# Performance work log

Hardware: AMD Instinct MI355X
Metric: run time of the kernel (lower is better)

## Reference

```python
import jax, jax.numpy as jnp
import numpy as np

B, S, H = 4, 256, 8
N_MB, N_C = 50000, 1000
P, BS, CS, L0, L1, L2 = 32, 16, 16, 96, 32, 16


def setup_inputs() -> dict:
    key = jax.random.key(0)
    ks = jax.random.split(key, 12)
    sd = 0.02
    return {
        "attention_scores": jax.random.normal(ks[0], (B, H, S, S), dtype=jnp.float32),
        "b_seq": jax.random.randint(ks[1], (B, S), 0, N_MB + 1, dtype=jnp.int32),
        "c_seq": jax.random.randint(ks[2], (B, S), 0, N_C + 2, dtype=jnp.int32),
        "e_pos": jax.random.normal(ks[3], (S * 2, H, P), dtype=jnp.float32) * sd,
        "e_bi": jax.random.normal(ks[4], (N_MB + 1, H, BS), dtype=jnp.float32) * sd,
        "e_bj": jax.random.normal(ks[5], (N_MB + 1, H, BS), dtype=jnp.float32) * sd,
        "e_ci": jax.random.normal(ks[6], (N_C + 2, H, CS), dtype=jnp.float32) * sd,
        "e_cj": jax.random.normal(ks[7], (N_C + 2, H, CS), dtype=jnp.float32) * sd,
        "w1_e": jax.random.normal(ks[8], (L0, L1, H), dtype=jnp.float32) * sd,
        "w2_e": jax.random.normal(ks[9], (L1, L2, H), dtype=jnp.float32) * sd,
        "w3_e": jax.random.normal(ks[10], (L2, H), dtype=jnp.float32) * sd,
    }


def reference(attention_scores, b_seq, c_seq, e_pos, e_bi, e_bj, e_ci, e_cj, w1_e, w2_e, w3_e):
    b, h, s, _ = attention_scores.shape
    pos = jnp.arange(s, dtype=jnp.int32)
    # relative position index (i - j + seq_len), shared across batch: [S,S]
    f_pos = pos[:, None] - pos[None, :] + s
    emb_pos = e_pos[f_pos]                 # [S,S,H,P]
    emb_bi = e_bi[b_seq]                   # [B,S,H,BS]
    emb_bj = e_bj[b_seq]
    emb_ci = e_ci[c_seq]                   # [B,S,H,CS]
    emb_cj = e_cj[c_seq]
    # concat of broadcasted features -> e: [B,S,S,H,L0]
    e = jnp.concatenate([
        jnp.broadcast_to(emb_pos[None], (b, s, s, h, emb_pos.shape[-1])),
        jnp.broadcast_to(emb_bi[:, :, None], (b, s, s, h, emb_bi.shape[-1])),
        jnp.broadcast_to(emb_bj[:, None, :], (b, s, s, h, emb_bj.shape[-1])),
        jnp.broadcast_to(emb_ci[:, :, None], (b, s, s, h, emb_ci.shape[-1])),
        jnp.broadcast_to(emb_cj[:, None, :], (b, s, s, h, emb_cj.shape[-1])),
    ], axis=-1)
    e1 = jax.nn.relu(jnp.einsum('bmnhd,dkh->bmnhk', e, w1_e))
    e2 = jax.nn.relu(jnp.einsum('bmnhk,klh->bmnhl', e1, w2_e))
    da_score = jnp.einsum('bmnhk,kh->bhmn', e2, w3_e)
    return attention_scores + da_score
```

## Files before the change

### kernel.cpp

```cpp
#include <hip/hip_runtime.h>
#include <stdint.h>

typedef __attribute__((ext_vector_type(8))) short short8;
typedef __attribute__((ext_vector_type(4))) float f32x4;

#define SEQ 256
#define NH 8

__device__ __forceinline__ uint32_t cvt_pk_bf16(float lo, float hi) {
  uint32_t r;
  asm("v_cvt_pk_bf16_f32 %0, %1, %2" : "=v"(r) : "v"(lo), "v"(hi));
  return r;
}

__device__ __forceinline__ short8 pack8(f32x4 a, f32x4 b) {
  union { uint32_t u[4]; short8 v; } t;
  t.u[0] = cvt_pk_bf16(a[0], a[1]);
  t.u[1] = cvt_pk_bf16(a[2], a[3]);
  t.u[2] = cvt_pk_bf16(b[0], b[1]);
  t.u[3] = cvt_pk_bf16(b[2], b[3]);
  return t.v;
}

__global__ __launch_bounds__(256) void build_tables_mfma(
    const int* __restrict__ bseq, const int* __restrict__ cseq,
    const float* __restrict__ epos, const float* __restrict__ ebi,
    const float* __restrict__ ebj, const float* __restrict__ eci,
    const float* __restrict__ ecj, const float* __restrict__ w1,
    float* __restrict__ Tpos, float* __restrict__ Ti, float* __restrict__ Tj) {
  int lane = threadIdx.x & 63, w = threadIdx.x >> 6;
  int task = blockIdx.x * 4 + w;
  int lcol = lane & 15, kb = lane >> 4, k8 = kb * 8;
  f32x4 zero = {0.f, 0.f, 0.f, 0.f};

  if (task < 256) {
    int h = task >> 5, ft = task & 31;
    short8 bf[2];
#pragma unroll
    for (int kt = 0; kt < 2; ++kt) {
      union { uint32_t u[4]; short8 v; } t;
#pragma unroll
      for (int r = 0; r < 4; ++r) {
        float lo = w1[(k8 + 2 * r) * 256 + (kt * 16 + lcol) * 8 + h];
        float hi = w1[(k8 + 2 * r + 1) * 256 + (kt * 16 + lcol) * 8 + h];
        t.u[r] = cvt_pk_bf16(lo, hi);
      }
      bf[kt] = t.v;
    }
    const float* ep = epos + ((ft * 16 + lcol) * NH + h) * 32 + k8;
    short8 af = pack8(*(const f32x4*)ep, *(const f32x4*)(ep + 4));
#pragma unroll
    for (int kt = 0; kt < 2; ++kt) {
      f32x4 d = __builtin_amdgcn_mfma_f32_16x16x32_bf16(af, bf[kt], zero, 0, 0, 0);
#pragma unroll
      for (int r = 0; r < 4; ++r)
        Tpos[h * 16384 + (ft * 16 + kb * 4 + r) * 32 + kt * 16 + lcol] = d[r];
    }
  } else {
    int isI = task < 768;
    int t2 = task - (isI ? 256 : 768);
    int h = t2 >> 6, bm = t2 & 63;
    int p0 = isI ? ((kb < 2 ? 32 : 48) + k8)
                 : ((kb < 2 ? 48 : 64) + k8);
    short8 bf[2];
#pragma unroll
    for (int kt = 0; kt < 2; ++kt) {
      union { uint32_t u[4]; short8 v; } t;
#pragma unroll
      for (int r = 0; r < 4; ++r) {
        float lo = w1[(p0 + 2 * r) * 256 + (kt * 16 + lcol) * 8 + h];
        float hi = w1[(p0 + 2 * r + 1) * 256 + (kt * 16 + lcol) * 8 + h];
        t.u[r] = cvt_pk_bf16(lo, hi);
      }
      bf[kt] = t.v;
    }
    int gm = bm * 16 + lcol;
    int bi = bseq[gm], ci = cseq[gm];
    const float* eB = isI ? ebi : ebj;
    const float* eC = isI ? eci : ecj;
    const float* src = (kb < 2) ? eB + (bi * NH + h) * 16 + k8
                                : eC + (ci * NH + h) * 16 + (k8 - 16);
    short8 af = pack8(*(const f32x4*)src, *(const f32x4*)(src + 4));
    float* T = isI ? Ti : Tj;
#pragma unroll
    for (int kt = 0; kt < 2; ++kt) {
      f32x4 d = __builtin_amdgcn_mfma_f32_16x16x32_bf16(af, bf[kt], zero, 0, 0, 0);
#pragma unroll
      for (int r = 0; r < 4; ++r)
        T[h * 32768 + (bm * 16 + kb * 4 + r) * 32 + kt * 16 + lcol] = d[r];
    }
  }
}

__global__ __launch_bounds__(512, 4) void dis_att_main(
    const float* __restrict__ attn, const float* __restrict__ w2,
    const float* __restrict__ w3, const float* __restrict__ Tpos,
    const float* __restrict__ Ti, const float* __restrict__ Tj,
    float* __restrict__ out) {
  __shared__ float sAp[127][36];
  __shared__ float sAi[64][36];
  __shared__ float sAj[64][36];
  int tid = threadIdx.x;
  int wg = blockIdx.x;
  int nt = wg & 3, mt = (wg >> 2) & 3, h = (wg >> 4) & 7, b = wg >> 7;
  int m0 = mt * 64, n0 = nt * 64;
  int f0 = m0 - n0 + 193;

  {
    int r = tid >> 3, q = tid & 7;
    const float* P = Tpos + h * 16384 + (f0 + r) * 32 + q * 4;
    *(f32x4*)&sAp[r][q * 4] = *(const f32x4*)P;
    if (r + 64 < 127)
      *(f32x4*)&sAp[r + 64][q * 4] = *(const f32x4*)(P + 64 * 32);
    *(f32x4*)&sAi[r][q * 4] =
        *(const f32x4*)(Ti + h * 32768 + (b * 256 + m0 + r) * 32 + q * 4);
    *(f32x4*)&sAj[r][q * 4] =
        *(const f32x4*)(Tj + h * 32768 + (b * 256 + n0 + r) * 32 + q * 4);
  }
  __syncthreads();

  int lane = tid & 63, w = tid >> 6;
  int lcol = lane & 15, kb = lane >> 4, k8 = kb * 8;
  f32x4 zero = {0.f, 0.f, 0.f, 0.f};

  union { uint32_t u[4]; short8 v; } w2f;
#pragma unroll
  for (int r = 0; r < 4; ++r) {
    float lo = w2[(k8 + 2 * r) * 128 + lcol * 8 + h];
    float hi = w2[(k8 + 2 * r + 1) * 128 + lcol * 8 + h];
    w2f.u[r] = cvt_pk_bf16(lo, hi);
  }
  float w3v[4];
#pragma unroll
  for (int r = 0; r < 4; ++r) w3v[r] = w3[(kb * 4 + r) * 8 + h];

  f32x4 ajA[4], ajB[4];
#pragma unroll
  for (int ng = 0; ng < 4; ++ng) {
    int nl = ng * 16 + lcol;
    ajA[ng] = *(const f32x4*)&sAj[nl][k8];
    ajB[ng] = *(const f32x4*)&sAj[nl][k8 + 4];
  }

  const float* attn_b = attn + (b * NH + h) * SEQ * SEQ;
  float* out_b = out + (b * NH + h) * SEQ * SEQ;
  int bit4 = kb & 1, bit5 = kb & 2;

#pragma unroll
  for (int s = 0; s < 2; ++s) {
    int mb = w * 8 + s * 4;
    float av[4];
    int idxs[4];
#pragma unroll
    for (int ng = 0; ng < 4; ++ng) {
      idxs[ng] = (m0 + mb + kb) * SEQ + n0 + ng * 16 + lcol;
      av[ng] = attn_b[idxs[ng]];
    }
    f32x4 aiA[4], aiB[4];
#pragma unroll
    for (int mi = 0; mi < 4; ++mi) {
      aiA[mi] = *(const f32x4*)&sAi[mb + mi][k8];
      aiB[mi] = *(const f32x4*)&sAi[mb + mi][k8 + 4];
    }
#pragma unroll
    for (int ng = 0; ng < 4; ++ng) {
      int nl = ng * 16 + lcol;
      f32x4 pA[4], pB[4];
#pragma unroll
      for (int mi = 0; mi < 4; ++mi) {
        int rl = mb + mi - nl + 63;
        pA[mi] = *(const f32x4*)&sAp[rl][k8];
        pB[mi] = *(const f32x4*)&sAp[rl][k8 + 4];
      }
      __builtin_amdgcn_sched_barrier(0);
      float part[4];
#pragma unroll
      for (int mi = 0; mi < 4; ++mi) {
        f32x4 s0 = pA[mi] + aiA[mi] + ajA[ng];
        f32x4 s1 = pB[mi] + aiB[mi] + ajB[ng];
        union { uint32_t u[4]; short8 v; } ef;
        ef.u[0] = cvt_pk_bf16(fmaxf(s0[0], 0.f), fmaxf(s0[1], 0.f));
        ef.u[1] = cvt_pk_bf16(fmaxf(s0[2], 0.f), fmaxf(s0[3], 0.f));
        ef.u[2] = cvt_pk_bf16(fmaxf(s1[0], 0.f), fmaxf(s1[1], 0.f));
        ef.u[3] = cvt_pk_bf16(fmaxf(s1[2], 0.f), fmaxf(s1[3], 0.f));
        f32x4 d = __builtin_amdgcn_mfma_f32_16x16x32_bf16(w2f.v, ef.v, zero, 0, 0, 0);
        part[mi] = fmaxf(d[0], 0.f) * w3v[0] + fmaxf(d[1], 0.f) * w3v[1] +
                   fmaxf(d[2], 0.f) * w3v[2] + fmaxf(d[3], 0.f) * w3v[3];
      }
      float mineA = bit4 ? part[1] : part[0];
      float sendA = bit4 ? part[0] : part[1];
      float mineB = bit4 ? part[3] : part[2];
      float sendB = bit4 ? part[2] : part[3];
      mineA += __shfl_xor(sendA, 16, 64);
      mineB += __shfl_xor(sendB, 16, 64);
      float keep = bit5 ? mineB : mineA;
      float send = bit5 ? mineA : mineB;
      float res = keep + __shfl_xor(send, 32, 64);
      out_b[idxs[ng]] = av[ng] + res;
    }
  }
}

extern "C" void kernel_launch(void* const* d_in, const int* in_sizes, int n_in,
                              void* d_out, int out_size, void* d_ws, size_t ws_size,
                              hipStream_t stream) {
  const float* attn = (const float*)d_in[0];
  const int* bseq   = (const int*)d_in[1];
  const int* cseq   = (const int*)d_in[2];
  const float* epos = (const float*)d_in[3];
  const float* ebi  = (const float*)d_in[4];
  const float* ebj  = (const float*)d_in[5];
  const float* eci  = (const float*)d_in[6];
  const float* ecj  = (const float*)d_in[7];
  const float* w1   = (const float*)d_in[8];
  const float* w2   = (const float*)d_in[9];
  const float* w3   = (const float*)d_in[10];
  float* out = (float*)d_out;

  float* Tpos = (float*)d_ws;
  float* Ti   = Tpos + 131072;
  float* Tj   = Ti + 262144;

  hipLaunchKernelGGL(build_tables_mfma, dim3(320), dim3(256), 0, stream,
                     bseq, cseq, epos, ebi, ebj, eci, ecj, w1, Tpos, Ti, Tj);
  hipLaunchKernelGGL(dis_att_main, dim3(512), dim3(512), 0, stream,
                     attn, w2, w3, Tpos, Ti, Tj, out);
}
```

Before: 25.66 us.

## Double-buffer positional LDS loads and use permlane swaps for lane reductions

Prefetches the next column group's positional table rows from LDS into a second register buffer while the current group's MFMAs run, replacing the sched_barrier that serialized the loads. The cross-lane reduction now uses permlane16/32 swap builtins, when available, to fully reduce each of the four partial sums instead of the select-and-shuffle scheme. Launch bounds are relaxed to 2 blocks per SM, allowing more registers for the extra buffer at the cost of occupancy. The full reductions do more adds and permutes per output than the previous butterfly scheme.

```diff
diff --git a/kernel.cpp b/kernel.cpp
--- a/kernel.cpp
+++ b/kernel.cpp
@@ -20,6 +20,27 @@
   t.u[2] = cvt_pk_bf16(b[0], b[1]);
   t.u[3] = cvt_pk_bf16(b[2], b[3]);
   return t.v;
+}
+
+__device__ __forceinline__ float xorsum16(float x) {
+#if __has_builtin(__builtin_amdgcn_permlane16_swap)
+  unsigned ux = __builtin_bit_cast(unsigned, x);
+  auto r = __builtin_amdgcn_permlane16_swap(ux, ux, false, false);
+  return __builtin_bit_cast(float, (unsigned)r[0]) +
+         __builtin_bit_cast(float, (unsigned)r[1]);
+#else
+  return x + __shfl_xor(x, 16, 64);
+#endif
+}
+__device__ __forceinline__ float xorsum32(float x) {
+#if __has_builtin(__builtin_amdgcn_permlane32_swap)
+  unsigned ux = __builtin_bit_cast(unsigned, x);
+  auto r = __builtin_amdgcn_permlane32_swap(ux, ux, false, false);
+  return __builtin_bit_cast(float, (unsigned)r[0]) +
+         __builtin_bit_cast(float, (unsigned)r[1]);
+#else
+  return x + __shfl_xor(x, 32, 64);
+#endif
 }
 
 __global__ __launch_bounds__(256) void build_tables_mfma(
@@ -92,7 +113,7 @@
   }
 }
 
-__global__ __launch_bounds__(512, 4) void dis_att_main(
+__global__ __launch_bounds__(512, 2) void dis_att_main(
     const float* __restrict__ attn, const float* __restrict__ w2,
     const float* __restrict__ w3, const float* __restrict__ Tpos,
     const float* __restrict__ Ti, const float* __restrict__ Tj,
@@ -162,22 +183,30 @@
       aiA[mi] = *(const f32x4*)&sAi[mb + mi][k8];
       aiB[mi] = *(const f32x4*)&sAi[mb + mi][k8 + 4];
     }
+    f32x4 pA[2][4], pB[2][4];
+#pragma unroll
+    for (int mi = 0; mi < 4; ++mi) {
+      int rl = mb + mi - lcol + 63;
+      pA[0][mi] = *(const f32x4*)&sAp[rl][k8];
+      pB[0][mi] = *(const f32x4*)&sAp[rl][k8 + 4];
+    }
 #pragma unroll
     for (int ng = 0; ng < 4; ++ng) {
-      int nl = ng * 16 + lcol;
-      f32x4 pA[4], pB[4];
+      int cur = ng & 1, nxt = cur ^ 1;
+      if (ng < 3) {
+        int nl2 = (ng + 1) * 16 + lcol;
+#pragma unroll
+        for (int mi = 0; mi < 4; ++mi) {
+          int rl = mb + mi - nl2 + 63;
+          pA[nxt][mi] = *(const f32x4*)&sAp[rl][k8];
+          pB[nxt][mi] = *(const f32x4*)&sAp[rl][k8 + 4];
+        }
+      }
+      float part[4];
 #pragma unroll
       for (int mi = 0; mi < 4; ++mi) {
-        int rl = mb + mi - nl + 63;
-        pA[mi] = *(const f32x4*)&sAp[rl][k8];
-        pB[mi] = *(const f32x4*)&sAp[rl][k8 + 4];
-      }
-      __builtin_amdgcn_sched_barrier(0);
-      float part[4];
-#pragma unroll
-      for (int mi = 0; mi < 4; ++mi) {
-        f32x4 s0 = pA[mi] + aiA[mi] + ajA[ng];
-        f32x4 s1 = pB[mi] + aiB[mi] + ajB[ng];
+        f32x4 s0 = pA[cur][mi] + aiA[mi] + ajA[ng];
+        f32x4 s1 = pB[cur][mi] + aiB[mi] + ajB[ng];
         union { uint32_t u[4]; short8 v; } ef;
         ef.u[0] = cvt_pk_bf16(fmaxf(s0[0], 0.f), fmaxf(s0[1], 0.f));
         ef.u[1] = cvt_pk_bf16(fmaxf(s0[2], 0.f), fmaxf(s0[3], 0.f));
@@ -187,16 +216,14 @@
         part[mi] = fmaxf(d[0], 0.f) * w3v[0] + fmaxf(d[1], 0.f) * w3v[1] +
                    fmaxf(d[2], 0.f) * w3v[2] + fmaxf(d[3], 0.f) * w3v[3];
       }
-      float mineA = bit4 ? part[1] : part[0];
-      float sendA = bit4 ? part[0] : part[1];
-      float mineB = bit4 ? part[3] : part[2];
-      float sendB = bit4 ? part[2] : part[3];
-      mineA += __shfl_xor(sendA, 16, 64);
-      mineB += __shfl_xor(sendB, 16, 64);
-      float keep = bit5 ? mineB : mineA;
-      float send = bit5 ? mineA : mineB;
-      float res = keep + __shfl_xor(send, 32, 64);
-      out_b[idxs[ng]] = av[ng] + res;
+      float S0 = xorsum32(xorsum16(part[0]));
+      float S1 = xorsum32(xorsum16(part[1]));
+      float S2 = xorsum32(xorsum16(part[2]));
+      float S3 = xorsum32(xorsum16(part[3]));
+      float p01 = bit4 ? S1 : S0;
+      float p23 = bit4 ? S3 : S2;
+      float pf = bit5 ? p23 : p01;
+      out_b[idxs[ng]] = av[ng] + pf;
     }
   }
 }
```

After: 28.70 us. 1.12x slower.

## Store first-layer tables as packed fp16 in LDS and use packed-half add/relu

Applied to the files above, without the earlier changes.

The main kernel now converts the precomputed position/i/j first-layer tables to fp16 when staging them into shared memory, which halves LDS footprint and read traffic. The per-element combine becomes packed f16 adds and a packed max instead of fp32 adds followed by bf16 conversion. The second-layer MFMA switches from bf16 to f16 inputs. This cuts VALU conversion work and LDS reads in the inner loop, at the cost of fp16 rounding and range in the summed hidden activations.

```diff
diff --git a/kernel.cpp b/kernel.cpp
--- a/kernel.cpp
+++ b/kernel.cpp
@@ -2,7 +2,9 @@
 #include <stdint.h>
 
 typedef __attribute__((ext_vector_type(8))) short short8;
+typedef __attribute__((ext_vector_type(8))) _Float16 half8;
 typedef __attribute__((ext_vector_type(4))) float f32x4;
+typedef __attribute__((ext_vector_type(4))) uint32_t u32x4;
 
 #define SEQ 256
 #define NH 8
@@ -10,6 +12,21 @@
 __device__ __forceinline__ uint32_t cvt_pk_bf16(float lo, float hi) {
   uint32_t r;
   asm("v_cvt_pk_bf16_f32 %0, %1, %2" : "=v"(r) : "v"(lo), "v"(hi));
+  return r;
+}
+__device__ __forceinline__ uint32_t cvt_pk_f16(float lo, float hi) {
+  uint32_t r;
+  asm("v_cvt_pkrtz_f16_f32 %0, %1, %2" : "=v"(r) : "v"(lo), "v"(hi));
+  return r;
+}
+__device__ __forceinline__ uint32_t pk_add(uint32_t a, uint32_t b) {
+  uint32_t r;
+  asm("v_pk_add_f16 %0, %1, %2" : "=v"(r) : "v"(a), "v"(b));
+  return r;
+}
+__device__ __forceinline__ uint32_t pk_relu(uint32_t a) {
+  uint32_t r;
+  asm("v_pk_max_f16 %0, %1, 0" : "=v"(r) : "v"(a));
   return r;
 }
 
@@ -97,9 +114,9 @@
     const float* __restrict__ w3, const float* __restrict__ Tpos,
     const float* __restrict__ Ti, const float* __restrict__ Tj,
     float* __restrict__ out) {
-  __shared__ float sAp[127][36];
-  __shared__ float sAi[64][36];
-  __shared__ float sAj[64][36];
+  __shared__ uint32_t sApB[127][20];
+  __shared__ uint32_t sAiB[64][20];
+  __shared__ uint32_t sAjB[64][20];
   int tid = threadIdx.x;
   int wg = blockIdx.x;
   int nt = wg & 3, mt = (wg >> 2) & 3, h = (wg >> 4) & 7, b = wg >> 7;
@@ -107,40 +124,54 @@
   int f0 = m0 - n0 + 193;
 
   {
-    int r = tid >> 3, q = tid & 7;
-    const float* P = Tpos + h * 16384 + (f0 + r) * 32 + q * 4;
-    *(f32x4*)&sAp[r][q * 4] = *(const f32x4*)P;
-    if (r + 64 < 127)
-      *(f32x4*)&sAp[r + 64][q * 4] = *(const f32x4*)(P + 64 * 32);
-    *(f32x4*)&sAi[r][q * 4] =
-        *(const f32x4*)(Ti + h * 32768 + (b * 256 + m0 + r) * 32 + q * 4);
-    *(f32x4*)&sAj[r][q * 4] =
-        *(const f32x4*)(Tj + h * 32768 + (b * 256 + n0 + r) * 32 + q * 4);
+    int r = tid >> 1, q = tid & 1;
+    const float* src = nullptr;
+    uint32_t* dst = nullptr;
+    if (r < 127) {
+      src = Tpos + h * 16384 + (f0 + r) * 32;
+      dst = &sApB[r][0];
+    } else if (r < 191) {
+      src = Ti + h * 32768 + (b * 256 + m0 + (r - 127)) * 32;
+      dst = &sAiB[r - 127][0];
+    } else if (r < 255) {
+      src = Tj + h * 32768 + (b * 256 + n0 + (r - 191)) * 32;
+      dst = &sAjB[r - 191][0];
+    }
+    if (src) {
+      const float* s16 = src + q * 16;
+      f32x4 v0 = *(const f32x4*)s16;
+      f32x4 v1 = *(const f32x4*)(s16 + 4);
+      f32x4 v2 = *(const f32x4*)(s16 + 8);
+      f32x4 v3 = *(const f32x4*)(s16 + 12);
+      u32x4 o0 = {cvt_pk_f16(v0[0], v0[1]), cvt_pk_f16(v0[2], v0[3]),
+                  cvt_pk_f16(v1[0], v1[1]), cvt_pk_f16(v1[2], v1[3])};
+      u32x4 o1 = {cvt_pk_f16(v2[0], v2[1]), cvt_pk_f16(v2[2], v2[3]),
+                  cvt_pk_f16(v3[0], v3[1]), cvt_pk_f16(v3[2], v3[3])};
+      *(u32x4*)(dst + q * 8) = o0;
+      *(u32x4*)(dst + q * 8 + 4) = o1;
+    }
   }
   __syncthreads();
 
   int lane = tid & 63, w = tid >> 6;
-  int lcol = lane & 15, kb = lane >> 4, k8 = kb * 8;
+  int lcol = lane & 15, kb = lane >> 4, k8 = kb * 8, kq = kb * 4;
   f32x4 zero = {0.f, 0.f, 0.f, 0.f};
 
-  union { uint32_t u[4]; short8 v; } w2f;
+  union { uint32_t u[4]; half8 v; } w2f;
 #pragma unroll
   for (int r = 0; r < 4; ++r) {
     float lo = w2[(k8 + 2 * r) * 128 + lcol * 8 + h];
     float hi = w2[(k8 + 2 * r + 1) * 128 + lcol * 8 + h];
-    w2f.u[r] = cvt_pk_bf16(lo, hi);
+    w2f.u[r] = cvt_pk_f16(lo, hi);
   }
   float w3v[4];
 #pragma unroll
   for (int r = 0; r < 4; ++r) w3v[r] = w3[(kb * 4 + r) * 8 + h];
 
-  f32x4 ajA[4], ajB[4];
-#pragma unroll
-  for (int ng = 0; ng < 4; ++ng) {
-    int nl = ng * 16 + lcol;
-    ajA[ng] = *(const f32x4*)&sAj[nl][k8];
-    ajB[ng] = *(const f32x4*)&sAj[nl][k8 + 4];
-  }
+  u32x4 ajP[4];
+#pragma unroll
+  for (int ng = 0; ng < 4; ++ng)
+    ajP[ng] = *(const u32x4*)&sAjB[ng * 16 + lcol][kq];
 
   const float* attn_b = attn + (b * NH + h) * SEQ * SEQ;
   float* out_b = out + (b * NH + h) * SEQ * SEQ;
@@ -156,34 +187,26 @@
       idxs[ng] = (m0 + mb + kb) * SEQ + n0 + ng * 16 + lcol;
       av[ng] = attn_b[idxs[ng]];
     }
-    f32x4 aiA[4], aiB[4];
-#pragma unroll
-    for (int mi = 0; mi < 4; ++mi) {
-      aiA[mi] = *(const f32x4*)&sAi[mb + mi][k8];
-      aiB[mi] = *(const f32x4*)&sAi[mb + mi][k8 + 4];
-    }
+    u32x4 aiP[4];
+#pragma unroll
+    for (int mi = 0; mi < 4; ++mi)
+      aiP[mi] = *(const u32x4*)&sAiB[mb + mi][kq];
 #pragma unroll
     for (int ng = 0; ng < 4; ++ng) {
       int nl = ng * 16 + lcol;
-      f32x4 pA[4], pB[4];
-#pragma unroll
-      for (int mi = 0; mi < 4; ++mi) {
-        int rl = mb + mi - nl + 63;
-        pA[mi] = *(const f32x4*)&sAp[rl][k8];
-        pB[mi] = *(const f32x4*)&sAp[rl][k8 + 4];
-      }
+      u32x4 pP[4];
+#pragma unroll
+      for (int mi = 0; mi < 4; ++mi)
+        pP[mi] = *(const u32x4*)&sApB[mb + mi - nl + 63][kq];
       __builtin_amdgcn_sched_barrier(0);
       float part[4];
 #pragma unroll
       for (int mi = 0; mi < 4; ++mi) {
-        f32x4 s0 = pA[mi] + aiA[mi] + ajA[ng];
-        f32x4 s1 = pB[mi] + aiB[mi] + ajB[ng];
-        union { uint32_t u[4]; short8 v; } ef;
-        ef.u[0] = cvt_pk_bf16(fmaxf(s0[0], 0.f), fmaxf(s0[1], 0.f));
-        ef.u[1] = cvt_pk_bf16(fmaxf(s0[2], 0.f), fmaxf(s0[3], 0.f));
-        ef.u[2] = cvt_pk_bf16(fmaxf(s1[0], 0.f), fmaxf(s1[1], 0.f));
-        ef.u[3] = cvt_pk_bf16(fmaxf(s1[2], 0.f), fmaxf(s1[3], 0.f));
-        f32x4 d = __builtin_amdgcn_mfma_f32_16x16x32_bf16(w2f.v, ef.v, zero, 0, 0, 0);
+        union { uint32_t u[4]; half8 v; } ef;
+#pragma unroll
+        for (int r = 0; r < 4; ++r)
+          ef.u[r] = pk_relu(pk_add(pk_add(pP[mi][r], aiP[mi][r]), ajP[ng][r]));
+        f32x4 d = __builtin_amdgcn_mfma_f32_16x16x32_f16(w2f.v, ef.v, zero, 0, 0, 0);
         part[mi] = fmaxf(d[0], 0.f) * w3v[0] + fmaxf(d[1], 0.f) * w3v[1] +
                    fmaxf(d[2], 0.f) * w3v[2] + fmaxf(d[3], 0.f) * w3v[3];
       }
```

Result: no change. 25.29 us (-1.4%).
